# Performance work log

Measured on AMD Instinct MI355X. Metric: run time of the kernel, lower is better.

## Reference

```python
import jax, jax.numpy as jnp
import numpy as np

N, E = 50000, 800000
MUL, NATTR, NEMB, HID, NPATH = 32, 8, 8, 8, 5
AVG_NEIGH = 16.0
INV3 = 1.0 / np.sqrt(3.0)  # CG norm for 1o x 1o -> 0e (dot)
INV2 = 1.0 / np.sqrt(2.0)  # CG norm for 1o x 1o -> 1o (cross)


def setup_inputs() -> dict:
    key = jax.random.key(0)
    ks = jax.random.split(key, 16)
    f = lambda k, s: jax.random.normal(k, s, jnp.float32)
    return {
        "node_s": f(ks[0], (N, MUL)),
        "node_v": f(ks[1], (N, MUL, 3)),
        "node_attrs": f(ks[2], (N, NATTR)),
        "edge_emb": f(ks[3], (E, NEMB)),
        "edge_sh0": f(ks[4], (E, 1)),
        "edge_sh1": f(ks[5], (E, 3)),
        "W1_s": f(ks[6], (MUL, MUL)),
        "W1_v": f(ks[7], (MUL, MUL)),
        "Wm1": f(ks[8], (NEMB, HID)),
        "Wm2": f(ks[9], (HID, NPATH * MUL)),
        "W2_s": f(ks[10], (2 * MUL, MUL)),
        "W2_v": f(ks[11], (3 * MUL, MUL)),
        "Wsc_s": f(ks[12], (MUL, NATTR, MUL)),
        "Wsc_v": f(ks[13], (MUL, NATTR, MUL)),
        "edge_src": jax.random.randint(ks[14], (E,), 0, N),
        "edge_dst": jax.random.randint(ks[15], (E,), 0, N),
    }


def reference(node_s, node_v, node_attrs, edge_emb, edge_sh0, edge_sh1,
              W1_s, W1_v, Wm1, Wm2, W2_s, W2_v, Wsc_s, Wsc_v,
              edge_src, edge_dst):
    # linear_1: per-l equivariant channel mixing
    x_s = node_s @ W1_s / np.sqrt(MUL)                          # [N, MUL]
    x_v = jnp.einsum('nuc,uv->nvc', node_v, W1_v) / np.sqrt(MUL)  # [N, MUL, 3]
    # gather source node features per edge
    s = x_s[edge_src]   # [E, MUL]
    v = x_v[edge_src]   # [E, MUL, 3]
    # radial MLP on edge embedding -> per-edge UVU tensor-product weights
    h = jax.nn.silu(edge_emb @ Wm1 / np.sqrt(NEMB))
    w = (h @ Wm2 / np.sqrt(HID)).reshape(E, NPATH, MUL)
    w1, w2, w3, w4, w5 = (w[:, i] for i in range(NPATH))
    # UVU Clebsch-Gordan paths (lmax = 1)
    p1 = w1 * s * edge_sh0                                              # 0e x 0e -> 0e
    p2 = w2 * jnp.einsum('euc,ec->eu', v, edge_sh1) * INV3              # 1o x 1o -> 0e
    p3 = w3[:, :, None] * s[:, :, None] * edge_sh1[:, None, :]          # 0e x 1o -> 1o
    p4 = w4[:, :, None] * v * edge_sh0[:, :, None]                      # 1o x 0e -> 1o
    p5 = w5[:, :, None] * jnp.cross(v, edge_sh1[:, None, :]) * INV2     # 1o x 1o -> 1o
    msg_s = jnp.concatenate([p1, p2], axis=1)       # [E, 2*MUL]
    msg_v = jnp.concatenate([p3, p4, p5], axis=1)   # [E, 3*MUL, 3]
    # scatter-add messages to destination nodes
    agg_s = jax.ops.segment_sum(msg_s, edge_dst, num_segments=N)
    agg_v = jax.ops.segment_sum(msg_v, edge_dst, num_segments=N)
    inv = 1.0 / np.sqrt(AVG_NEIGH)
    agg_s = agg_s * inv
    agg_v = agg_v * inv
    # linear_2
    m_s = agg_s @ W2_s / np.sqrt(2 * MUL)
    m_v = jnp.einsum('nuc,uv->nvc', agg_v, W2_v) / np.sqrt(3 * MUL)
    # self connection: fully connected TP with scalar node attrs
    nsc = 1.0 / np.sqrt(MUL * NATTR)
    sc_s = jnp.einsum('nu,na,uav->nv', node_s, node_attrs, Wsc_s) * nsc
    sc_v = jnp.einsum('nuc,na,uav->nvc', node_v, node_attrs, Wsc_v) * nsc
    out_s = m_s + sc_s                  # [N, MUL]
    out_v = m_v + sc_v                  # [N, MUL, 3]
    return jnp.concatenate([out_s, out_v.reshape(N, MUL * 3)], axis=1)  # [N, 128]
```

## Files before the change

kernel.cpp:

```cpp
#include <hip/hip_runtime.h>
#include <math.h>

#define NN 50000
#define NE 800000
#define MUL 32
#define NPB 4
#define SCANB 49

static __device__ __forceinline__ float sigmoidf_(float v) {
    return 1.0f / (1.0f + __expf(-v));
}

#define INV_SQRT_MUL   0.17677669529663687f
#define INV_SQRT_NEMB  0.35355339059327373f
#define INV_SQRT_HID   0.35355339059327373f
#define INV3C          0.5773502691896258f
#define INV2C          0.7071067811865476f
#define INV_NEIGH      0.25f
#define INV_SQRT_2MUL  0.125f
#define INV_SQRT_3MUL  0.10206207261596575f
#define NSC            0.0625f

__global__ __launch_bounds__(256) void k_node(
    const float* __restrict__ node_s, const float* __restrict__ node_v,
    const float* __restrict__ attrs,
    const float* __restrict__ W1_s, const float* __restrict__ W1_v,
    const float* __restrict__ Wsc_s, const float* __restrict__ Wsc_v,
    const int* __restrict__ edge_dst, int* __restrict__ counts,
    float* __restrict__ x, float* __restrict__ out)
{
    __shared__ float nd[NPB][136];
    __shared__ float gs[NPB][1024];
    __shared__ float gv[NPB][1024];
    const int t  = threadIdx.x;
    const int nb = blockIdx.x * NPB;

    {
        int g = blockIdx.x * 256 + t;
        if (g < NE) atomicAdd(&counts[edge_dst[g]], 1);
    }

#pragma unroll
    for (int i = t; i < NPB * 128; i += 256) {
        int nn = i >> 7, j = i & 127;
        nd[nn][j] = (j < 32) ? node_s[(nb + nn) * 32 + j]
                             : node_v[(nb + nn) * 96 + (j - 32)];
    }
    if (t < NPB * 8) nd[t >> 3][128 + (t & 7)] = attrs[(nb + (t >> 3)) * 8 + (t & 7)];
    __syncthreads();

    float at[NPB][8];
#pragma unroll
    for (int nn = 0; nn < NPB; ++nn)
#pragma unroll
        for (int a = 0; a < 8; ++a) at[nn][a] = nd[nn][128 + a];

#pragma unroll
    for (int r = 0; r < 4; ++r) {
        const int idx = t + 256 * r;
        const int u = idx >> 5, vch = idx & 31;
        float as[NPB] = {0.f, 0.f, 0.f, 0.f};
        float av[NPB] = {0.f, 0.f, 0.f, 0.f};
#pragma unroll
        for (int a = 0; a < 8; ++a) {
            const float ws = Wsc_s[(u * 8 + a) * 32 + vch];
            const float wv = Wsc_v[(u * 8 + a) * 32 + vch];
#pragma unroll
            for (int nn = 0; nn < NPB; ++nn) {
                as[nn] += at[nn][a] * ws;
                av[nn] += at[nn][a] * wv;
            }
        }
#pragma unroll
        for (int nn = 0; nn < NPB; ++nn) {
            gs[nn][idx] = as[nn];
            gv[nn][idx] = av[nn];
        }
    }
    __syncthreads();

    const int o  = t & 127;
    const int nh = t >> 7;
    if (o < 32) {
        float ax[2] = {0.f, 0.f}, asc[2] = {0.f, 0.f};
#pragma unroll
        for (int uu = 0; uu < 32; ++uu) {
            const float w1 = W1_s[uu * 32 + o];
#pragma unroll
            for (int r2 = 0; r2 < 2; ++r2) {
                const int nn = nh + 2 * r2;
                const float s = nd[nn][uu];
                ax[r2]  += s * w1;
                asc[r2] += s * gs[nn][(uu << 5) + o];
            }
        }
#pragma unroll
        for (int r2 = 0; r2 < 2; ++r2) {
            const int nidx = nb + nh + 2 * r2;
            x[(size_t)nidx * 128 + 4 * o] = ax[r2] * INV_SQRT_MUL;
            out[(size_t)nidx * 128 + o]   = asc[r2] * NSC;
        }
    } else {
        const int q = o - 32;
        const int vch = q / 3, c = q - 3 * vch;
        float ax[2] = {0.f, 0.f}, asc[2] = {0.f, 0.f};
#pragma unroll
        for (int uu = 0; uu < 32; ++uu) {
            const float w1 = W1_v[uu * 32 + vch];
#pragma unroll
            for (int r2 = 0; r2 < 2; ++r2) {
                const int nn = nh + 2 * r2;
                const float vv = nd[nn][32 + 3 * uu + c];
                ax[r2]  += vv * w1;
                asc[r2] += vv * gv[nn][(uu << 5) + vch];
            }
        }
#pragma unroll
        for (int r2 = 0; r2 < 2; ++r2) {
            const int nidx = nb + nh + 2 * r2;
            x[(size_t)nidx * 128 + 4 * vch + 1 + c] = ax[r2] * INV_SQRT_MUL;
            out[(size_t)nidx * 128 + o]             = asc[r2] * NSC;
        }
    }
}

__global__ __launch_bounds__(1024) void k_scan_a(
    const int* __restrict__ counts, int* __restrict__ escan,
    int* __restrict__ bsum)
{
    __shared__ int sh[1024];
    const int t = threadIdx.x;
    const int i = blockIdx.x * 1024 + t;
    int v = (i < NN) ? counts[i] : 0;
    sh[t] = v;
    __syncthreads();
    for (int off = 1; off < 1024; off <<= 1) {
        int u = (t >= off) ? sh[t - off] : 0;
        __syncthreads();
        sh[t] += u;
        __syncthreads();
    }
    if (i < NN) escan[i] = sh[t] - v;
    if (t == 1023) bsum[blockIdx.x] = sh[1023];
}

__global__ __launch_bounds__(1024) void k_scan_c(
    const int* __restrict__ escan, const int* __restrict__ bsum,
    int* __restrict__ offsets, int* __restrict__ cursor)
{
    __shared__ int sbase;
    const int t = threadIdx.x;
    if (t < 64) {
        int v = (t < blockIdx.x) ? bsum[t] : 0;
        for (int off = 32; off > 0; off >>= 1) v += __shfl_xor(v, off, 64);
        if (t == 0) sbase = v;
    }
    __syncthreads();
    const int i = blockIdx.x * 1024 + t;
    if (i == 0) offsets[NN] = NE;
    if (i < NN) {
        int o = sbase + escan[i];
        offsets[i] = o;
        cursor[i] = o;
    }
}

__global__ __launch_bounds__(256) void k_pack(
    const float* __restrict__ edge_emb, const float* __restrict__ edge_sh0,
    const float* __restrict__ edge_sh1,
    const int* __restrict__ edge_src, const int* __restrict__ edge_dst,
    const float* __restrict__ Wm1,
    int* __restrict__ cursor, float* __restrict__ epack)
{
    int e = blockIdx.x * 256 + threadIdx.x;
    if (e >= NE) return;
    const float4* p = (const float4*)(edge_emb + e * 8);
    float4 a = p[0], b = p[1];
    float emb[8] = {a.x, a.y, a.z, a.w, b.x, b.y, b.z, b.w};
    float h[8];
#pragma unroll
    for (int j = 0; j < 8; ++j) {
        float s = 0.f;
#pragma unroll
        for (int k = 0; k < 8; ++k) s += emb[k] * Wm1[k * 8 + j];
        s *= INV_SQRT_NEMB;
        h[j] = s * sigmoidf_(s);
    }
    float sh0 = edge_sh0[e];
    float sx = edge_sh1[3 * e], sy = edge_sh1[3 * e + 1], sz = edge_sh1[3 * e + 2];
    int src = edge_src[e];
    int pos = atomicAdd(&cursor[edge_dst[e]], 1);
    float4* op = (float4*)(epack + (size_t)pos * 16);
    op[0] = make_float4(__int_as_float(src), sh0, sx, sy);
    op[1] = make_float4(sz, h[0], h[1], h[2]);
    op[2] = make_float4(h[3], h[4], h[5], h[6]);
    op[3] = make_float4(h[7], 0.f, 0.f, 0.f);
}

__global__ __launch_bounds__(64) void k_gather(
    const float* __restrict__ x, const float* __restrict__ epack,
    const float* __restrict__ Wm2, const float* __restrict__ W2_s,
    const float* __restrict__ W2_v,
    const int* __restrict__ offsets, float* __restrict__ out)
{
    __shared__ float msg[352];
    const int n = blockIdx.x;
    const int L = threadIdx.x;
    const int u = L & 31;
    const int role = L >> 5;

    float wc[3][8];
#pragma unroll
    for (int p = 0; p < 3; ++p) {
        int m = (role == 0 ? p : 3 + p) * 32 + u;
        if (m > 159) m = u;
#pragma unroll
        for (int q = 0; q < 8; ++q) wc[p][q] = Wm2[q * 160 + m];
    }

    float a0 = 0.f, a1 = 0.f;
    float b0 = 0.f, b1 = 0.f, b2 = 0.f;
    float c0 = 0.f, c1 = 0.f, c2 = 0.f;

    const int beg = offsets[n];
    const int end = offsets[n + 1];

    if (end > beg) {
        const float4* rp = (const float4*)(epack + (size_t)beg * 16);
        float4 r0 = rp[0];
        float4 r1 = rp[1];
        float4 r2 = rp[2];
        float  h7 = epack[(size_t)beg * 16 + 12];
        float4 xv = *(const float4*)(x + (size_t)__float_as_int(r0.x) * 128 + 4 * u);

        for (int e = beg; e < end; ++e) {
            const int ip = (e + 1 < end) ? (e + 1) : e;
            const float4* np = (const float4*)(epack + (size_t)ip * 16);
            const float4 q0 = np[0];
            const float4 q1 = np[1];
            const float4 q2 = np[2];
            const float  qh7 = epack[(size_t)ip * 16 + 12];
            const float4 nxv = *(const float4*)(x + (size_t)__float_as_int(q0.x) * 128 + 4 * u);

            const float sh0 = r0.y, sx = r0.z, sy = r0.w, sz = r1.x;
            float w0 = r1.y * wc[0][0] + r1.z * wc[0][1] + r1.w * wc[0][2]
                     + r2.x * wc[0][3] + r2.y * wc[0][4] + r2.z * wc[0][5]
                     + r2.w * wc[0][6] + h7  * wc[0][7];
            float w1 = r1.y * wc[1][0] + r1.z * wc[1][1] + r1.w * wc[1][2]
                     + r2.x * wc[1][3] + r2.y * wc[1][4] + r2.z * wc[1][5]
                     + r2.w * wc[1][6] + h7  * wc[1][7];
            float w2 = r1.y * wc[2][0] + r1.z * wc[2][1] + r1.w * wc[2][2]
                     + r2.x * wc[2][3] + r2.y * wc[2][4] + r2.z * wc[2][5]
                     + r2.w * wc[2][6] + h7  * wc[2][7];
            w0 *= INV_SQRT_HID; w1 *= INV_SQRT_HID; w2 *= INV_SQRT_HID;

            const float ls = xv.x, lv0 = xv.y, lv1 = xv.z, lv2 = xv.w;
            if (role == 0) {
                a0 += w0 * ls * sh0;
                a1 += w1 * (lv0 * sx + lv1 * sy + lv2 * sz);
                float tt = w2 * ls;
                b0 += tt * sx; b1 += tt * sy; b2 += tt * sz;
            } else {
                float t4 = w0 * sh0;
                b0 += t4 * lv0; b1 += t4 * lv1; b2 += t4 * lv2;
                c0 += w1 * (lv1 * sz - lv2 * sy);
                c1 += w1 * (lv2 * sx - lv0 * sz);
                c2 += w1 * (lv0 * sy - lv1 * sx);
            }
            r0 = q0; r1 = q1; r2 = q2; h7 = qh7;
            xv = nxv;
        }
    }

    if (role == 0) {
        msg[u]      = a0 * INV_NEIGH;
        msg[32 + u] = a1 * (INV3C * INV_NEIGH);
        int vb = 64 + u * 3;
        msg[vb]     = b0 * INV_NEIGH;
        msg[vb + 1] = b1 * INV_NEIGH;
        msg[vb + 2] = b2 * INV_NEIGH;
    } else {
        int vb4 = 64 + (32 + u) * 3;
        msg[vb4]     = b0 * INV_NEIGH;
        msg[vb4 + 1] = b1 * INV_NEIGH;
        msg[vb4 + 2] = b2 * INV_NEIGH;
        int vb5 = 64 + (64 + u) * 3;
        float f = INV2C * INV_NEIGH;
        msg[vb5]     = c0 * f;
        msg[vb5 + 1] = c1 * f;
        msg[vb5 + 2] = c2 * f;
    }
    __syncthreads();

#pragma unroll
    for (int oo = 0; oo < 2; ++oo) {
        int o = oo * 64 + L;
        float r;
        if (o < 32) {
            float s = 0.f;
#pragma unroll
            for (int uu = 0; uu < 64; ++uu) s += msg[uu] * W2_s[uu * 32 + o];
            r = s * INV_SQRT_2MUL;
        } else {
            int q = o - 32;
            int vch = q / 3, c = q - 3 * vch;
            float s = 0.f;
#pragma unroll
            for (int uu = 0; uu < 96; ++uu) s += msg[64 + uu * 3 + c] * W2_v[uu * 32 + vch];
            r = s * INV_SQRT_3MUL;
        }
        out[128 * n + o] += r;
    }
}

extern "C" void kernel_launch(void* const* d_in, const int* in_sizes, int n_in,
                              void* d_out, int out_size, void* d_ws, size_t ws_size,
                              hipStream_t stream) {
    const float* node_s   = (const float*)d_in[0];
    const float* node_v   = (const float*)d_in[1];
    const float* attrs    = (const float*)d_in[2];
    const float* edge_emb = (const float*)d_in[3];
    const float* edge_sh0 = (const float*)d_in[4];
    const float* edge_sh1 = (const float*)d_in[5];
    const float* W1_s     = (const float*)d_in[6];
    const float* W1_v     = (const float*)d_in[7];
    const float* Wm1      = (const float*)d_in[8];
    const float* Wm2      = (const float*)d_in[9];
    const float* W2_s     = (const float*)d_in[10];
    const float* W2_v     = (const float*)d_in[11];
    const float* Wsc_s    = (const float*)d_in[12];
    const float* Wsc_v    = (const float*)d_in[13];
    const int*   edge_src = (const int*)d_in[14];
    const int*   edge_dst = (const int*)d_in[15];
    float* out = (float*)d_out;

    float* x     = (float*)d_ws;
    float* epack = x + (size_t)NN * 128;
    int*   counts  = (int*)(epack + (size_t)NE * 16);
    int*   offsets = counts + NN;
    int*   cursor  = offsets + NN + 1;
    int*   escan   = cursor + NN;
    int*   bsum    = escan + NN;

    hipMemsetAsync(counts, 0, NN * sizeof(int), stream);

    k_node<<<NN / NPB, 256, 0, stream>>>(node_s, node_v, attrs,
                                         W1_s, W1_v, Wsc_s, Wsc_v,
                                         edge_dst, counts, x, out);
    k_scan_a<<<SCANB, 1024, 0, stream>>>(counts, escan, bsum);
    k_scan_c<<<SCANB, 1024, 0, stream>>>(escan, bsum, offsets, cursor);
    k_pack<<<(NE + 255) / 256, 256, 0, stream>>>(edge_emb, edge_sh0, edge_sh1,
                                                 edge_src, edge_dst, Wm1,
                                                 cursor, epack);
    k_gather<<<NN, 64, 0, stream>>>(x, epack, Wm2, W2_s, W2_v, offsets, out);
}
```

Measured before the change: 416.9 us.

## Split edges across half-waves and batch four nodes per gather block

The gather kernel now handles four nodes per 256-thread block, one wave per node. Each half-wave covers alternating edges and computes all five paths, and the halves are combined with a cross-lane shuffle instead of each half owning fixed paths over every edge. This halves the serial edge-loop length per node, which was latency-bound on dependent gathers. W2 weights are staged in shared memory and shared by the four nodes, and the message layout is made component-major so the output linear reads stride-1. The cost is more registers (40 Wm2 coefficients per thread) and a 20KB+ shared footprint, which may reduce occupancy.

```diff
diff --git a/kernel.cpp b/kernel.cpp
--- a/kernel.cpp
+++ b/kernel.cpp
@@ -64,11 +64,11 @@
 #pragma unroll
         for (int a = 0; a < 8; ++a) {
             const float ws = Wsc_s[(u * 8 + a) * 32 + vch];
-            const float wv = Wsc_v[(u * 8 + a) * 32 + vch];
+            const float wvw = Wsc_v[(u * 8 + a) * 32 + vch];
 #pragma unroll
             for (int nn = 0; nn < NPB; ++nn) {
                 as[nn] += at[nn][a] * ws;
-                av[nn] += at[nn][a] * wv;
+                av[nn] += at[nn][a] * wvw;
             }
         }
 #pragma unroll
@@ -197,119 +197,145 @@
     op[3] = make_float4(h[7], 0.f, 0.f, 0.f);
 }
 
-__global__ __launch_bounds__(64) void k_gather(
+__global__ __launch_bounds__(256) void k_gather(
     const float* __restrict__ x, const float* __restrict__ epack,
     const float* __restrict__ Wm2, const float* __restrict__ W2_s,
     const float* __restrict__ W2_v,
     const int* __restrict__ offsets, float* __restrict__ out)
 {
-    __shared__ float msg[352];
-    const int n = blockIdx.x;
-    const int L = threadIdx.x;
-    const int u = L & 31;
-    const int role = L >> 5;
-
-    float wc[3][8];
-#pragma unroll
-    for (int p = 0; p < 3; ++p) {
-        int m = (role == 0 ? p : 3 + p) * 32 + u;
-        if (m > 159) m = u;
-#pragma unroll
-        for (int q = 0; q < 8; ++q) wc[p][q] = Wm2[q * 160 + m];
-    }
-
-    float a0 = 0.f, a1 = 0.f;
-    float b0 = 0.f, b1 = 0.f, b2 = 0.f;
-    float c0 = 0.f, c1 = 0.f, c2 = 0.f;
+    __shared__ __align__(16) float wsh[2048];
+    __shared__ __align__(16) float wvh[3072];
+    __shared__ float msg[4][360];
+
+    for (int i = threadIdx.x; i < 512; i += 256)
+        ((float4*)wsh)[i] = ((const float4*)W2_s)[i];
+    for (int i = threadIdx.x; i < 768; i += 256)
+        ((float4*)wvh)[i] = ((const float4*)W2_v)[i];
+
+    const int w    = threadIdx.x >> 6;
+    const int L    = threadIdx.x & 63;
+    const int u    = L & 31;
+    const int half = L >> 5;
+    const int n    = blockIdx.x * 4 + w;
+
+    float wc[5][8];
+#pragma unroll
+    for (int p = 0; p < 5; ++p)
+#pragma unroll
+        for (int q = 0; q < 8; ++q)
+            wc[p][q] = Wm2[q * 160 + p * 32 + u] * INV_SQRT_HID;
+
+    float pa = 0.f, pb = 0.f;
+    float p30 = 0.f, p31 = 0.f, p32 = 0.f;
+    float p40 = 0.f, p41 = 0.f, p42 = 0.f;
+    float p50 = 0.f, p51 = 0.f, p52 = 0.f;
 
     const int beg = offsets[n];
     const int end = offsets[n + 1];
-
-    if (end > beg) {
-        const float4* rp = (const float4*)(epack + (size_t)beg * 16);
-        float4 r0 = rp[0];
-        float4 r1 = rp[1];
-        float4 r2 = rp[2];
-        float  h7 = epack[(size_t)beg * 16 + 12];
+    const int cnt = end - beg;
+
+#define EDGE_BODY() do { \
+        const float sh0 = r0.y, sx = r0.z, sy = r0.w, sz = r1.x; \
+        const float w0 = r1.y*wc[0][0] + r1.z*wc[0][1] + r1.w*wc[0][2] + r2.x*wc[0][3] \
+                       + r2.y*wc[0][4] + r2.z*wc[0][5] + r2.w*wc[0][6] + h7*wc[0][7]; \
+        const float w1 = r1.y*wc[1][0] + r1.z*wc[1][1] + r1.w*wc[1][2] + r2.x*wc[1][3] \
+                       + r2.y*wc[1][4] + r2.z*wc[1][5] + r2.w*wc[1][6] + h7*wc[1][7]; \
+        const float w2 = r1.y*wc[2][0] + r1.z*wc[2][1] + r1.w*wc[2][2] + r2.x*wc[2][3] \
+                       + r2.y*wc[2][4] + r2.z*wc[2][5] + r2.w*wc[2][6] + h7*wc[2][7]; \
+        const float w3 = r1.y*wc[3][0] + r1.z*wc[3][1] + r1.w*wc[3][2] + r2.x*wc[3][3] \
+                       + r2.y*wc[3][4] + r2.z*wc[3][5] + r2.w*wc[3][6] + h7*wc[3][7]; \
+        const float w4 = r1.y*wc[4][0] + r1.z*wc[4][1] + r1.w*wc[4][2] + r2.x*wc[4][3] \
+                       + r2.y*wc[4][4] + r2.z*wc[4][5] + r2.w*wc[4][6] + h7*wc[4][7]; \
+        const float ls = xv.x, lv0 = xv.y, lv1 = xv.z, lv2 = xv.w; \
+        pa += w0 * (ls * sh0); \
+        pb += w1 * (lv0 * sx + lv1 * sy + lv2 * sz); \
+        const float t2 = w2 * ls; \
+        p30 += t2 * sx; p31 += t2 * sy; p32 += t2 * sz; \
+        const float t3 = w3 * sh0; \
+        p40 += t3 * lv0; p41 += t3 * lv1; p42 += t3 * lv2; \
+        p50 += w4 * (lv1 * sz - lv2 * sy); \
+        p51 += w4 * (lv2 * sx - lv0 * sz); \
+        p52 += w4 * (lv0 * sy - lv1 * sx); \
+    } while (0)
+
+    if (cnt > 0) {
+        int e = beg + half;
+        int le = min(e, end - 1);
+        const float4* rp = (const float4*)(epack + (size_t)le * 16);
+        float4 r0 = rp[0], r1 = rp[1], r2 = rp[2];
+        float  h7 = epack[(size_t)le * 16 + 12];
         float4 xv = *(const float4*)(x + (size_t)__float_as_int(r0.x) * 128 + 4 * u);
 
-        for (int e = beg; e < end; ++e) {
-            const int ip = (e + 1 < end) ? (e + 1) : e;
-            const float4* np = (const float4*)(epack + (size_t)ip * 16);
-            const float4 q0 = np[0];
-            const float4 q1 = np[1];
-            const float4 q2 = np[2];
-            const float  qh7 = epack[(size_t)ip * 16 + 12];
+        const int np = cnt >> 1;
+        for (int it = 0; it < np; ++it) {
+            const int pe = min(e + 2, end - 1);
+            const float4* qp = (const float4*)(epack + (size_t)pe * 16);
+            const float4 q0 = qp[0], q1 = qp[1], q2 = qp[2];
+            const float  qh7 = epack[(size_t)pe * 16 + 12];
             const float4 nxv = *(const float4*)(x + (size_t)__float_as_int(q0.x) * 128 + 4 * u);
 
-            const float sh0 = r0.y, sx = r0.z, sy = r0.w, sz = r1.x;
-            float w0 = r1.y * wc[0][0] + r1.z * wc[0][1] + r1.w * wc[0][2]
-                     + r2.x * wc[0][3] + r2.y * wc[0][4] + r2.z * wc[0][5]
-                     + r2.w * wc[0][6] + h7  * wc[0][7];
-            float w1 = r1.y * wc[1][0] + r1.z * wc[1][1] + r1.w * wc[1][2]
-                     + r2.x * wc[1][3] + r2.y * wc[1][4] + r2.z * wc[1][5]
-                     + r2.w * wc[1][6] + h7  * wc[1][7];
-            float w2 = r1.y * wc[2][0] + r1.z * wc[2][1] + r1.w * wc[2][2]
-                     + r2.x * wc[2][3] + r2.y * wc[2][4] + r2.z * wc[2][5]
-                     + r2.w * wc[2][6] + h7  * wc[2][7];
-            w0 *= INV_SQRT_HID; w1 *= INV_SQRT_HID; w2 *= INV_SQRT_HID;
-
-            const float ls = xv.x, lv0 = xv.y, lv1 = xv.z, lv2 = xv.w;
-            if (role == 0) {
-                a0 += w0 * ls * sh0;
-                a1 += w1 * (lv0 * sx + lv1 * sy + lv2 * sz);
-                float tt = w2 * ls;
-                b0 += tt * sx; b1 += tt * sy; b2 += tt * sz;
-            } else {
-                float t4 = w0 * sh0;
-                b0 += t4 * lv0; b1 += t4 * lv1; b2 += t4 * lv2;
-                c0 += w1 * (lv1 * sz - lv2 * sy);
-                c1 += w1 * (lv2 * sx - lv0 * sz);
-                c2 += w1 * (lv0 * sy - lv1 * sx);
+            EDGE_BODY();
+
+            r0 = q0; r1 = q1; r2 = q2; h7 = qh7; xv = nxv;
+            e += 2;
+        }
+        if (cnt & 1) {
+            const float mask = (half == 0) ? 1.f : 0.f;
+            r0.y *= mask; r0.z *= mask; r0.w *= mask; r1.x *= mask;
+            EDGE_BODY();
+        }
+    }
+#undef EDGE_BODY
+
+    pa  += __shfl_xor(pa, 32);  pb  += __shfl_xor(pb, 32);
+    p30 += __shfl_xor(p30, 32); p31 += __shfl_xor(p31, 32); p32 += __shfl_xor(p32, 32);
+    p40 += __shfl_xor(p40, 32); p41 += __shfl_xor(p41, 32); p42 += __shfl_xor(p42, 32);
+    p50 += __shfl_xor(p50, 32); p51 += __shfl_xor(p51, 32); p52 += __shfl_xor(p52, 32);
+
+    {
+        float* mg = msg[w];
+        if (half == 0) {
+            mg[u]              = pa  * INV_NEIGH;
+            mg[32 + u]         = pb  * (INV3C * INV_NEIGH);
+            mg[64 + u]         = p30 * INV_NEIGH;
+            mg[64 + 96 + u]    = p31 * INV_NEIGH;
+            mg[64 + 192 + u]   = p32 * INV_NEIGH;
+        } else {
+            mg[64 + 32 + u]        = p40 * INV_NEIGH;
+            mg[64 + 96 + 32 + u]   = p41 * INV_NEIGH;
+            mg[64 + 192 + 32 + u]  = p42 * INV_NEIGH;
+            const float f = INV2C * INV_NEIGH;
+            mg[64 + 64 + u]        = p50 * f;
+            mg[64 + 96 + 64 + u]   = p51 * f;
+            mg[64 + 192 + 64 + u]  = p52 * f;
+        }
+    }
+    __syncthreads();
+
+    {
+        const int nb = blockIdx.x * 4;
+        const int t = threadIdx.x;
+        if (t < 128) {
+            const int node = t >> 5, o = t & 31;
+            float s = 0.f;
+#pragma unroll
+            for (int uu = 0; uu < 64; ++uu) s += msg[node][uu] * wsh[uu * 32 + o];
+            out[(size_t)(nb + node) * 128 + o] += s * INV_SQRT_2MUL;
+        } else {
+            const int node = (t - 128) >> 5, vch = t & 31;
+            float s0 = 0.f, s1 = 0.f, s2 = 0.f;
+#pragma unroll
+            for (int uu = 0; uu < 96; ++uu) {
+                const float wgt = wvh[uu * 32 + vch];
+                s0 += msg[node][64 + uu]       * wgt;
+                s1 += msg[node][64 + 96 + uu]  * wgt;
+                s2 += msg[node][64 + 192 + uu] * wgt;
             }
-            r0 = q0; r1 = q1; r2 = q2; h7 = qh7;
-            xv = nxv;
-        }
-    }
-
-    if (role == 0) {
-        msg[u]      = a0 * INV_NEIGH;
-        msg[32 + u] = a1 * (INV3C * INV_NEIGH);
-        int vb = 64 + u * 3;
-        msg[vb]     = b0 * INV_NEIGH;
-        msg[vb + 1] = b1 * INV_NEIGH;
-        msg[vb + 2] = b2 * INV_NEIGH;
-    } else {
-        int vb4 = 64 + (32 + u) * 3;
-        msg[vb4]     = b0 * INV_NEIGH;
-        msg[vb4 + 1] = b1 * INV_NEIGH;
-        msg[vb4 + 2] = b2 * INV_NEIGH;
-        int vb5 = 64 + (64 + u) * 3;
-        float f = INV2C * INV_NEIGH;
-        msg[vb5]     = c0 * f;
-        msg[vb5 + 1] = c1 * f;
-        msg[vb5 + 2] = c2 * f;
-    }
-    __syncthreads();
-
-#pragma unroll
-    for (int oo = 0; oo < 2; ++oo) {
-        int o = oo * 64 + L;
-        float r;
-        if (o < 32) {
-            float s = 0.f;
-#pragma unroll
-            for (int uu = 0; uu < 64; ++uu) s += msg[uu] * W2_s[uu * 32 + o];
-            r = s * INV_SQRT_2MUL;
-        } else {
-            int q = o - 32;
-            int vch = q / 3, c = q - 3 * vch;
-            float s = 0.f;
-#pragma unroll
-            for (int uu = 0; uu < 96; ++uu) s += msg[64 + uu * 3 + c] * W2_v[uu * 32 + vch];
-            r = s * INV_SQRT_3MUL;
-        }
-        out[128 * n + o] += r;
+            float* po = out + (size_t)(nb + node) * 128 + 32 + vch * 3;
+            po[0] += s0 * INV_SQRT_3MUL;
+            po[1] += s1 * INV_SQRT_3MUL;
+            po[2] += s2 * INV_SQRT_3MUL;
+        }
     }
 }
 
@@ -352,5 +378,6 @@
     k_pack<<<(NE + 255) / 256, 256, 0, stream>>>(edge_emb, edge_sh0, edge_sh1,
                                                  edge_src, edge_dst, Wm1,
                                                  cursor, epack);
-    k_gather<<<NN, 64, 0, stream>>>(x, epack, Wm2, W2_s, W2_v, offsets, out);
-}
+    k_gather<<<NN / 4, 256, 0, stream>>>(x, epack, Wm2, W2_s, W2_v,
+                                         offsets, out);
+}
```

After: 411.7 us. About the same (-1.2%).
